# Kernel optimization log

Measured on AMD Instinct MI355X. Metric: run time of the kernel, lower is better.

Reference implementation:

```python
import jax, jax.numpy as jnp
import numpy as np

D_MODEL = 1024
D_STATE = 8          # max(8, 16 // 2)
D_CONV = 4
D_INNER = int(1.5 * D_MODEL)   # expand = max(1.5, 2*0.75)
DT_RANK = (D_MODEL + 15) // 16 # 64
D_FF = 2 * D_MODEL
B, L = 2, 2048


def layer_norm(x, g, b, eps=1e-5):
    mu = jnp.mean(x, -1, keepdims=True)
    var = jnp.var(x, -1, keepdims=True)
    return (x - mu) * jax.lax.rsqrt(var + eps) * g + b


def setup_inputs() -> dict:
    key = jax.random.key(0)
    ks = jax.random.split(key, 12)
    def n(k, shape, scale=0.02):
        return jax.random.normal(k, shape, dtype=jnp.float32) * scale
    return {
        'x': jax.random.normal(ks[0], (B, L, D_MODEL), dtype=jnp.float32),
        'ln1_g': jnp.ones((D_MODEL,), jnp.float32),
        'ln1_b': jnp.zeros((D_MODEL,), jnp.float32),
        'ln2_g': jnp.ones((D_MODEL,), jnp.float32),
        'ln2_b': jnp.zeros((D_MODEL,), jnp.float32),
        'in_proj_w': n(ks[1], (2 * D_INNER, D_MODEL)),
        'conv_w': n(ks[2], (D_INNER, 1, D_CONV), 0.1),
        'conv_b': jnp.zeros((D_INNER,), jnp.float32),
        'x_proj_w': n(ks[3], (DT_RANK + 2 * D_STATE, D_INNER)),
        'dt_proj_w': n(ks[4], (D_INNER, DT_RANK), 0.1),
        'dt_proj_b': n(ks[5], (D_INNER,), 0.1),
        'A_log': jnp.log(jnp.broadcast_to(jnp.arange(1, D_STATE + 1, dtype=jnp.float32), (D_INNER, D_STATE))),
        'D': jnp.ones((D_INNER,), jnp.float32),
        'out_proj_w': n(ks[6], (D_MODEL, D_INNER)),
        'ffn_w1': n(ks[7], (D_FF, D_MODEL)),
        'ffn_b1': jnp.zeros((D_FF,), jnp.float32),
        'ffn_w2': n(ks[8], (D_MODEL, D_FF)),
        'ffn_b2': jnp.zeros((D_MODEL,), jnp.float32),
    }


def mamba(x, in_proj_w, conv_w, conv_b, x_proj_w, dt_proj_w, dt_proj_b, A_log, Dp, out_proj_w):
    # in_proj -> (x, z)
    xz = x @ in_proj_w.T                       # (B, L, 2*d_inner)
    xi, z = jnp.split(xz, 2, axis=-1)
    # depthwise causal conv over seq, kernel 4
    xc = jnp.transpose(xi, (0, 2, 1))          # (B, d_inner, L)
    xc = jax.lax.conv_general_dilated(
        xc, conv_w, window_strides=(1,), padding=[(D_CONV - 1, 0)],
        dimension_numbers=('NCH', 'OIH', 'NCH'), feature_group_count=D_INNER)
    xc = xc + conv_b[None, :, None]
    u = jax.nn.silu(jnp.transpose(xc, (0, 2, 1)))  # (B, L, d_inner)
    # x_proj -> dt, B, C
    x_dbl = u @ x_proj_w.T
    dt = x_dbl[..., :DT_RANK]
    Bm = x_dbl[..., DT_RANK:DT_RANK + D_STATE]
    Cm = x_dbl[..., DT_RANK + D_STATE:]
    delta = jax.nn.softplus(dt @ dt_proj_w.T + dt_proj_b)  # (B, L, d_inner)
    A = -jnp.exp(A_log)                                    # (d_inner, d_state)
    dA = jnp.exp(jnp.einsum('bld,dn->bldn', delta, A))     # (B, L, d_inner, d_state)
    dBu = jnp.einsum('bld,bln,bld->bldn', delta, Bm, u)
    # selective scan over time
    def step(h, inputs):
        dA_t, dBu_t, C_t = inputs
        h = dA_t * h + dBu_t                   # (B, d_inner, d_state)
        y = jnp.einsum('bdn,bn->bd', h, C_t)
        return h, y
    h0 = jnp.zeros((x.shape[0], D_INNER, D_STATE), x.dtype)
    _, ys = jax.lax.scan(step, h0, (jnp.moveaxis(dA, 1, 0), jnp.moveaxis(dBu, 1, 0), jnp.moveaxis(Cm, 1, 0)))
    y = jnp.moveaxis(ys, 0, 1) + u * Dp        # skip connection D*u
    y = y * jax.nn.silu(z)                     # gate
    return y @ out_proj_w.T


def reference(x, ln1_g, ln1_b, ln2_g, ln2_b, in_proj_w, conv_w, conv_b, x_proj_w,
              dt_proj_w, dt_proj_b, A_log, D, out_proj_w, ffn_w1, ffn_b1, ffn_w2, ffn_b2):
    residual = x
    xp = layer_norm(x, ln1_g, ln1_b)
    x = mamba(xp, in_proj_w, conv_w, conv_b, x_proj_w, dt_proj_w, dt_proj_b, A_log, D, out_proj_w) + residual
    xn = layer_norm(x, ln2_g, ln2_b)
    h = jax.nn.gelu(xn @ ffn_w1.T + ffn_b1, approximate=False)  # dropout is identity in eval
    return x + (h @ ffn_w2.T + ffn_b2)
```

## Files before the change

kernel.cpp:

```cpp
#include <hip/hip_runtime.h>
#include <math.h>

#define D_MODEL 1024
#define D_STATE 8
#define D_CONV  4
#define D_INNER 1536
#define DT_RANK 64
#define D_FF    2048
#define BATCH   2
#define SEQ     2048
#define NROWS   (BATCH*SEQ)
#define NC      32
#define LC      (SEQ/NC)
#define XQW     512

typedef short bf16x8 __attribute__((ext_vector_type(8)));
typedef unsigned short u16x8 __attribute__((ext_vector_type(8)));
typedef float f32x4  __attribute__((ext_vector_type(4)));

__device__ inline unsigned short f2bf(float x) {
    union { float f; unsigned u; } v; v.f = x;
    unsigned r = v.u + 0x7fffu + ((v.u >> 16) & 1u);
    return (unsigned short)(r >> 16);
}
__device__ inline float bf2f(unsigned short h) {
    union { unsigned u; float f; } v; v.u = ((unsigned)h) << 16;
    return v.f;
}
__device__ inline float softplus_f(float x) {
    return (x > 20.0f) ? x : log1pf(__expf(x));
}
__device__ inline float gelu_f(float x) {
    return 0.5f * x * (1.0f + erff(x * 0.70710678118654752f));
}
__device__ inline float silu_f(float x) {
    return x / (1.0f + __expf(-x));
}
__device__ inline void gload16(const unsigned short* g, unsigned short* l) {
    typedef unsigned int u32;
    __builtin_amdgcn_global_load_lds(
        (const __attribute__((address_space(1))) u32*)g,
        (__attribute__((address_space(3))) u32*)l, 16, 0, 0);
}

#define PHASE_SYNC_PRE()  do { __builtin_amdgcn_s_barrier(); \
                               asm volatile("s_waitcnt lgkmcnt(0)" ::: "memory"); } while (0)
#define PHASE_SYNC_POST() do { __builtin_amdgcn_s_barrier(); } while (0)

__global__ __launch_bounds__(256) void prep_kernel(
    const float* __restrict__ s0, unsigned short* __restrict__ d0,
    const float* __restrict__ s1, unsigned short* __restrict__ d1,
    const float* __restrict__ s2, unsigned short* __restrict__ d2,
    const float* __restrict__ s3, unsigned short* __restrict__ d3,
    const float* __restrict__ s4, unsigned short* __restrict__ d4,
    const float* __restrict__ xpw, unsigned short* __restrict__ xpd,
    const float* __restrict__ x, const float* __restrict__ g1,
    const float* __restrict__ b1, unsigned short* __restrict__ xout) {
    int b = blockIdx.x;
    if (b < 4400) {
        const float* s; unsigned short* d; int base;
        if      (b < 1536) { s = s0; d = d0; base = b * 2048; }
        else if (b < 1584) { s = s1; d = d1; base = (b - 1536) * 2048; }
        else if (b < 2352) { s = s2; d = d2; base = (b - 1584) * 2048; }
        else if (b < 3376) { s = s3; d = d3; base = (b - 2352) * 2048; }
        else               { s = s4; d = d4; base = (b - 3376) * 2048; }
        int i = base + threadIdx.x * 8;
        float4 v0 = *(const float4*)(s + i);
        float4 v1 = *(const float4*)(s + i + 4);
        ushort4 a, c;
        a.x = f2bf(v0.x); a.y = f2bf(v0.y); a.z = f2bf(v0.z); a.w = f2bf(v0.w);
        c.x = f2bf(v1.x); c.y = f2bf(v1.y); c.z = f2bf(v1.z); c.w = f2bf(v1.w);
        *(ushort4*)(d + i)     = a;
        *(ushort4*)(d + i + 4) = c;
    } else if (b < 4528) {
        int row = b - 4400;
        for (int c = threadIdx.x; c < D_INNER; c += 256)
            xpd[row * D_INNER + c] = (row < 80) ? f2bf(xpw[row * D_INNER + c]) : (unsigned short)0;
    } else {
        __shared__ float sbuf[4];
        int row = b - 4528;
        int t = threadIdx.x;
        float4 v = ((const float4*)(x + (size_t)row * D_MODEL))[t];
        float s = v.x + v.y + v.z + v.w;
        for (int o = 32; o; o >>= 1) s += __shfl_down(s, o, 64);
        if ((t & 63) == 0) sbuf[t >> 6] = s;
        __syncthreads();
        float mu = (sbuf[0] + sbuf[1] + sbuf[2] + sbuf[3]) * (1.0f / D_MODEL);
        __syncthreads();
        float e0 = v.x - mu, e1 = v.y - mu, e2 = v.z - mu, e3 = v.w - mu;
        float q = e0*e0 + e1*e1 + e2*e2 + e3*e3;
        for (int o = 32; o; o >>= 1) q += __shfl_down(q, o, 64);
        if ((t & 63) == 0) sbuf[t >> 6] = q;
        __syncthreads();
        float var = (sbuf[0] + sbuf[1] + sbuf[2] + sbuf[3]) * (1.0f / D_MODEL);
        float rs = rsqrtf(var + 1e-5f);
        float4 gv = ((const float4*)g1)[t];
        float4 bv = ((const float4*)b1)[t];
        ushort4 st;
        st.x = f2bf(e0 * rs * gv.x + bv.x);
        st.y = f2bf(e1 * rs * gv.y + bv.y);
        st.z = f2bf(e2 * rs * gv.z + bv.z);
        st.w = f2bf(e3 * rs * gv.w + bv.w);
        ((ushort4*)(xout + (size_t)row * D_MODEL))[t] = st;
    }
}

#define EPI_F32        0
#define EPI_GELU_BF16  4
#define EPI_BF16       6
#define EPI_SOFTPLUS_BF16 7
#define EPI_PBF16      9

template<int WN, int EPI, int SPLITK>
__global__ __launch_bounds__(512, 2) void gemm8p(
    const unsigned short* __restrict__ A, int lda,
    const unsigned short* __restrict__ Bm, int ldb, int K,
    float* __restrict__ Cf, unsigned short* __restrict__ Cb, int ldc,
    const float* __restrict__ bias,
    const float* __restrict__ resid, int ldr) {
    constexpr int WM = 8 / WN;
    constexpr int BN = WN * 64;
    constexpr int RW = 256 / WM;
    constexpr int CW = 64;
    constexpr int MI = RW / 16;
    constexpr int NI = CW / 16;
    constexpr int MIH = MI / 2, NIH = NI / 2;
    constexpr int ABYTES = 256 * 128;
    constexpr int BBYTES = BN * 128;
    constexpr int BOFF = 2 * ABYTES;
    __shared__ unsigned short lds[(2 * ABYTES + 2 * BBYTES) / 2];

    const int t = threadIdx.x, l = t & 63, w = t >> 6;
    const int wr = w / WN, wc = w % WN;

    const int nx = gridDim.x;
    const int nwg = nx * gridDim.y;
    int bid = blockIdx.y * nx + blockIdx.x;
    int q = nwg >> 3;
    int swz = (bid & 7) * q + (bid >> 3);
    const int m0 = (swz / nx) * 256, n0 = (swz % nx) * BN;
    const int kbase = (SPLITK > 1) ? blockIdx.z * K : 0;

    const int sr = l >> 3;
    const int sj = ((l & 7) * 16) ^ ((l >> 3) << 4);
    const int row_l = w * 8;
    const int row_c = (w >> 2) * 64 + (w & 3) * 8;

    auto STG = [&](int bufbyte, int rowbase, const unsigned short* G, int ldg, int gbase, int kt) {
        unsigned short* dst = (unsigned short*)((char*)lds + bufbyte + rowbase * 128);
        const unsigned short* src = G + (size_t)(gbase + rowbase + sr) * ldg + kbase + kt * 64 + (sj >> 1);
        gload16(src, dst);
    };
    auto S_Ah0 = [&](int b, int kt) {
        if (WN == 4) { STG(b * ABYTES, row_l, A, lda, m0, kt);       STG(b * ABYTES, 128 + row_l, A, lda, m0, kt); }
        else         { STG(b * ABYTES, row_c, A, lda, m0, kt);       STG(b * ABYTES, 128 + row_c, A, lda, m0, kt); }
    };
    auto S_Ah1 = [&](int b, int kt) {
        if (WN == 4) { STG(b * ABYTES, 64 + row_l, A, lda, m0, kt);  STG(b * ABYTES, 192 + row_l, A, lda, m0, kt); }
        else         { STG(b * ABYTES, 32 + row_c, A, lda, m0, kt);  STG(b * ABYTES, 160 + row_c, A, lda, m0, kt); }
    };
    auto S_Bc0 = [&](int b, int kt) {
        if (WN == 4) { STG(BOFF + b * BBYTES, row_c, Bm, ldb, n0, kt); STG(BOFF + b * BBYTES, 128 + row_c, Bm, ldb, n0, kt); }
        else         { STG(BOFF + b * BBYTES, row_c, Bm, ldb, n0, kt); }
    };
    auto S_Bc1 = [&](int b, int kt) {
        if (WN == 4) { STG(BOFF + b * BBYTES, 32 + row_c, Bm, ldb, n0, kt); STG(BOFF + b * BBYTES, 160 + row_c, Bm, ldb, n0, kt); }
        else         { STG(BOFF + b * BBYTES, 32 + row_c, Bm, ldb, n0, kt); }
    };

    auto LD = [&](int bytebase, int row, int kb) -> bf16x8 {
        int o = bytebase + row * 128 + (kb ^ ((row & 7) << 4));
        return *(const bf16x8*)((const char*)lds + o);
    };

    f32x4 acc[MI][NI] = {};
    bf16x8 af[MIH][2], b0v[NIH][2], b1v[NIH][2];

    auto LDA_set = [&](int buf, int qr, auto& dst) {
        #pragma unroll
        for (int mi = 0; mi < MIH; mi++)
            #pragma unroll
            for (int ks = 0; ks < 2; ks++)
                dst[mi][ks] = LD(buf * ABYTES, wr * RW + qr * (RW / 2) + mi * 16 + (l & 15),
                                 ks * 64 + (l >> 4) * 16);
    };
    auto LDB_set = [&](int buf, int qc, auto& dst) {
        #pragma unroll
        for (int ni2 = 0; ni2 < NIH; ni2++)
            #pragma unroll
            for (int ks = 0; ks < 2; ks++)
                dst[ni2][ks] = LD(BOFF + buf * BBYTES, wc * CW + qc * 32 + ni2 * 16 + (l & 15),
                                  ks * 64 + (l >> 4) * 16);
    };
    auto MFMA_Q = [&](int qr, int qc, auto& a_, auto& b_) {
        __builtin_amdgcn_s_setprio(1);
        #pragma unroll
        for (int mi = 0; mi < MIH; mi++)
            #pragma unroll
            for (int ni2 = 0; ni2 < NIH; ni2++)
                #pragma unroll
                for (int ks = 0; ks < 2; ks++)
                    acc[qr * MIH + mi][qc * NIH + ni2] =
                        __builtin_amdgcn_mfma_f32_16x16x32_bf16(a_[mi][ks], b_[ni2][ks],
                                                                acc[qr * MIH + mi][qc * NIH + ni2], 0, 0, 0);
        __builtin_amdgcn_s_setprio(0);
    };
    auto VMW = [&](bool last) {
        if (last)            asm volatile("s_waitcnt vmcnt(0)" ::: "memory");
        else if (WN == 4)    asm volatile("s_waitcnt vmcnt(6)" ::: "memory");
        else                 asm volatile("s_waitcnt vmcnt(5)" ::: "memory");
    };

    const int ni_ = K >> 7;

    S_Ah0(0, 0); S_Ah1(0, 0); S_Bc0(0, 0); S_Bc1(0, 0);
    S_Ah0(1, 1); S_Ah1(1, 1); S_Bc0(1, 1); S_Bc1(1, 1);
    if (WN == 4) asm volatile("s_waitcnt vmcnt(8)" ::: "memory");
    else         asm volatile("s_waitcnt vmcnt(6)" ::: "memory");
    __builtin_amdgcn_s_barrier();

    for (int i = 0; i < ni_; i++) {
        const bool last = (i == ni_ - 1);
        const int t2 = 2 * i + 2, t3 = 2 * i + 3;
        LDA_set(0, 0, af); LDB_set(0, 0, b0v);
        if (i) S_Bc0(1, 2 * i + 1);
        PHASE_SYNC_PRE(); MFMA_Q(0, 0, af, b0v); PHASE_SYNC_POST();
        LDB_set(0, 1, b1v);
        if (!last) S_Ah0(0, t2);
        PHASE_SYNC_PRE(); MFMA_Q(0, 1, af, b1v); PHASE_SYNC_POST();
        LDA_set(0, 1, af);
        PHASE_SYNC_PRE(); MFMA_Q(1, 1, af, b1v); PHASE_SYNC_POST();
        LDB_set(0, 0, b0v);
        if (!last) { S_Ah1(0, t2); S_Bc1(0, t2); }
        VMW(last);
        PHASE_SYNC_PRE(); MFMA_Q(1, 0, af, b0v); PHASE_SYNC_POST();
        LDA_set(1, 0, af); LDB_set(1, 0, b0v);
        if (!last) S_Bc0(0, t2);
        PHASE_SYNC_PRE(); MFMA_Q(0, 0, af, b0v); PHASE_SYNC_POST();
        LDB_set(1, 1, b1v);
        if (!last) S_Ah0(1, t3);
        PHASE_SYNC_PRE(); MFMA_Q(0, 1, af, b1v); PHASE_SYNC_POST();
        LDA_set(1, 1, af);
        PHASE_SYNC_PRE(); MFMA_Q(1, 1, af, b1v); PHASE_SYNC_POST();
        LDB_set(1, 0, b0v);
        if (!last) { S_Ah1(1, t3); S_Bc1(1, t3); }
        VMW(last);
        PHASE_SYNC_PRE(); MFMA_Q(1, 0, af, b0v); PHASE_SYNC_POST();
    }

    float* Cfp = Cf;
    unsigned short* Cbp = Cb;
    if (SPLITK > 1) {
        Cfp += (size_t)blockIdx.z * NROWS * ldc;
        Cbp += (size_t)blockIdx.z * NROWS * ldc;
    }
    #pragma unroll
    for (int ni2 = 0; ni2 < NI; ni2++) {
        int col = n0 + wc * CW + ni2 * 16 + (l & 15);
        float bv = 0.0f;
        if (EPI == EPI_GELU_BF16) bv = bias[col];
        #pragma unroll
        for (int mi = 0; mi < MI; mi++) {
            #pragma unroll
            for (int j = 0; j < 4; j++) {
                int row = m0 + wr * RW + mi * 16 + (l >> 4) * 4 + j;
                float v = acc[mi][ni2][j];
                if (EPI == EPI_GELU_BF16)  v = gelu_f(v + bv);
                if (EPI == EPI_GELU_BF16 || EPI == EPI_BF16 || EPI == EPI_PBF16) {
                    Cbp[(size_t)row * ldc + col] = f2bf(v);
                } else {
                    Cfp[(size_t)row * ldc + col] = v;
                }
            }
        }
    }
}

__global__ __launch_bounds__(256) void sk2_ln(const unsigned short* __restrict__ p,
                                              const float* __restrict__ resid,
                                              const float* __restrict__ g,
                                              const float* __restrict__ b,
                                              float* __restrict__ x2,
                                              unsigned short* __restrict__ xn) {
    __shared__ float sbuf[4];
    int row = blockIdx.x;
    int t = threadIdx.x;
    const size_t seg = (size_t)NROWS * D_MODEL;
    size_t base = (size_t)row * D_MODEL + t * 4;
    ushort4 a = *(const ushort4*)(p + base);
    ushort4 bb = *(const ushort4*)(p + base + seg);
    float4 r = *(const float4*)(resid + base);
    float4 v;
    v.x = bf2f(a.x) + bf2f(bb.x) + r.x;
    v.y = bf2f(a.y) + bf2f(bb.y) + r.y;
    v.z = bf2f(a.z) + bf2f(bb.z) + r.z;
    v.w = bf2f(a.w) + bf2f(bb.w) + r.w;
    *(float4*)(x2 + base) = v;
    float s = v.x + v.y + v.z + v.w;
    for (int o = 32; o; o >>= 1) s += __shfl_down(s, o, 64);
    if ((t & 63) == 0) sbuf[t >> 6] = s;
    __syncthreads();
    float mu = (sbuf[0] + sbuf[1] + sbuf[2] + sbuf[3]) * (1.0f / D_MODEL);
    __syncthreads();
    float d0 = v.x - mu, d1 = v.y - mu, d2 = v.z - mu, d3 = v.w - mu;
    float qq = d0*d0 + d1*d1 + d2*d2 + d3*d3;
    for (int o = 32; o; o >>= 1) qq += __shfl_down(qq, o, 64);
    if ((t & 63) == 0) sbuf[t >> 6] = qq;
    __syncthreads();
    float var = (sbuf[0] + sbuf[1] + sbuf[2] + sbuf[3]) * (1.0f / D_MODEL);
    float rs = rsqrtf(var + 1e-5f);
    float4 gv = ((const float4*)g)[t];
    float4 bv = ((const float4*)b)[t];
    ushort4 st;
    st.x = f2bf(d0 * rs * gv.x + bv.x);
    st.y = f2bf(d1 * rs * gv.y + bv.y);
    st.z = f2bf(d2 * rs * gv.z + bv.z);
    st.w = f2bf(d3 * rs * gv.w + bv.w);
    ((ushort4*)(xn + (size_t)row * D_MODEL))[t] = st;
}

__global__ __launch_bounds__(256) void sk2_reduce(const unsigned short* __restrict__ p,
                                                  const float* __restrict__ bias,
                                                  const float* __restrict__ resid,
                                                  float* __restrict__ o) {
    int i = (blockIdx.x * 256 + threadIdx.x) * 4;
    const size_t seg = (size_t)NROWS * D_MODEL;
    ushort4 a = *(const ushort4*)(p + i);
    ushort4 b = *(const ushort4*)(p + i + seg);
    float4 r = *(const float4*)(resid + i);
    float4 bb = *(const float4*)(bias + (i & (D_MODEL - 1)));
    float4 o4;
    o4.x = bf2f(a.x) + bf2f(b.x) + r.x + bb.x;
    o4.y = bf2f(a.y) + bf2f(b.y) + r.y + bb.y;
    o4.z = bf2f(a.z) + bf2f(b.z) + r.z + bb.z;
    o4.w = bf2f(a.w) + bf2f(b.w) + r.w + bb.w;
    *(float4*)(o + i) = o4;
}

__global__ __launch_bounds__(256) void xproj_conv_gemm(
    const unsigned short* __restrict__ xz, const float* __restrict__ cw,
    const float* __restrict__ cb, unsigned short* __restrict__ u,
    const unsigned short* __restrict__ B,
    unsigned short* __restrict__ xq) {
    __shared__ unsigned short As[128 * 32];
    __shared__ unsigned short Bs[128 * 32];
    int t = threadIdx.x, l = t & 63, w = t >> 6;
    int m0 = blockIdx.x * 128;
    int kbase = blockIdx.y * 384;
    int c0 = 2 * w, c1 = 2 * w + 1;
    int srow = l >> 2, scol = (l & 3) * 8;
    const unsigned short* Bg0 = B + (size_t)(16 * c0 + srow) * D_INNER + kbase + scol;
    const unsigned short* Bg1 = B + (size_t)(16 * c1 + srow) * D_INNER + kbase + scol;
    int wr = w >> 1, wc = w & 1;
    int aoff = (wr * 64 + (l & 15)) * 32 + (l >> 4) * 8;
    int boff = (wc * 64 + (l & 15)) * 32 + (l >> 4) * 8;

    f32x4 acc[4][4] = {};

    for (int ti = 0; ti < 12; ti++) {
        int k0 = ti * 32;
        gload16(Bg0 + k0, &Bs[c0 * 512]);
        gload16(Bg1 + k0, &Bs[c1 * 512]);
        #pragma unroll
        for (int cc = 0; cc < 2; cc++) {
            int ch = 2 * w + cc;
            int bl = m0 + 16 * ch + srow;
            int d0 = kbase + k0 + scol;
            int lq = bl & (SEQ - 1);
            u16x8 rr[4];
            #pragma unroll
            for (int kk = 0; kk < 4; kk++) {
                if (lq - 3 + kk >= 0)
                    rr[kk] = *(const u16x8*)(xz + (size_t)(bl - 3 + kk) * (2 * D_INNER) + d0);
                else
                    rr[kk] = (u16x8)0;
            }
            float4 cb0 = *(const float4*)(cb + d0);
            float4 cb1 = *(const float4*)(cb + d0 + 4);
            float av[8];
            av[0] = cb0.x; av[1] = cb0.y; av[2] = cb0.z; av[3] = cb0.w;
            av[4] = cb1.x; av[5] = cb1.y; av[6] = cb1.z; av[7] = cb1.w;
            u16x8 o;
            #pragma unroll
            for (int j = 0; j < 8; j++) {
                float4 wv = *(const float4*)(cw + (d0 + j) * 4);
                float s = av[j];
                s += bf2f((unsigned short)rr[0][j]) * wv.x;
                s += bf2f((unsigned short)rr[1][j]) * wv.y;
                s += bf2f((unsigned short)rr[2][j]) * wv.z;
                s += bf2f((unsigned short)rr[3][j]) * wv.w;
                o[j] = f2bf(silu_f(s));
            }
            *(u16x8*)(&As[ch * 512 + l * 8]) = o;
            *(u16x8*)(u + (size_t)bl * D_INNER + d0) = o;
        }
        __syncthreads();
        bf16x8 af[4], bfv[4];
        #pragma unroll
        for (int i = 0; i < 4; i++) af[i] = *(const bf16x8*)(&As[aoff + i * 512]);
        #pragma unroll
        for (int i = 0; i < 4; i++) bfv[i] = *(const bf16x8*)(&Bs[boff + i * 512]);
        __builtin_amdgcn_s_setprio(1);
        #pragma unroll
        for (int mi = 0; mi < 4; mi++)
            #pragma unroll
            for (int ni = 0; ni < 4; ni++)
                acc[mi][ni] = __builtin_amdgcn_mfma_f32_16x16x32_bf16(af[mi], bfv[ni], acc[mi][ni], 0, 0, 0);
        __builtin_amdgcn_s_setprio(0);
        __syncthreads();
    }

    unsigned short* Cb = xq + blockIdx.y * 128;
    int colb = wc * 64 + (l & 15);
    int rowb = m0 + wr * 64 + (l >> 4) * 4;
    #pragma unroll
    for (int ni = 0; ni < 4; ni++) {
        int col = colb + ni * 16;
        #pragma unroll
        for (int mi = 0; mi < 4; mi++) {
            #pragma unroll
            for (int j = 0; j < 4; j++) {
                int row = rowb + mi * 16 + j;
                Cb[(size_t)row * XQW + col] = f2bf(acc[mi][ni][j]);
            }
        }
    }
}

__global__ __launch_bounds__(256) void xdt_reduce(const unsigned short* __restrict__ xq,
                                                  unsigned short* __restrict__ xdt) {
    int i = blockIdx.x * 256 + threadIdx.x;
    int row = i >> 4;
    int c = (i & 15) * 4;
    const unsigned short* xr = xq + (size_t)row * XQW + c;
    ushort4 a0 = *(const ushort4*)(xr);
    ushort4 a1 = *(const ushort4*)(xr + 128);
    ushort4 a2 = *(const ushort4*)(xr + 256);
    ushort4 a3 = *(const ushort4*)(xr + 384);
    ushort4 o;
    o.x = f2bf(bf2f(a0.x) + bf2f(a1.x) + bf2f(a2.x) + bf2f(a3.x));
    o.y = f2bf(bf2f(a0.y) + bf2f(a1.y) + bf2f(a2.y) + bf2f(a3.y));
    o.z = f2bf(bf2f(a0.z) + bf2f(a1.z) + bf2f(a2.z) + bf2f(a3.z));
    o.w = f2bf(bf2f(a0.w) + bf2f(a1.w) + bf2f(a2.w) + bf2f(a3.w));
    *(ushort4*)(xdt + (size_t)row * DT_RANK + c) = o;
}

template<int EPI>
__global__ __launch_bounds__(256) void gemm_mfma(
    const unsigned short* __restrict__ A, int lda,
    const unsigned short* __restrict__ B, int ldb, int K,
    float* __restrict__ Cf, unsigned short* __restrict__ Cb, int ldc,
    const float* __restrict__ bias) {
    __shared__ unsigned short As[3][128 * 32];
    __shared__ unsigned short Bs[3][128 * 32];
    int t = threadIdx.x, l = t & 63, w = t >> 6;
    int nx = gridDim.x;
    int nwg = nx * gridDim.y;
    int bid = blockIdx.y * nx + blockIdx.x;
    int q = nwg >> 3;
    int swz = (bid & 7) * q + (bid >> 3);
    int m0 = (swz / nx) * 128, n0 = (swz % nx) * 128;
    int c0 = 2 * w, c1 = 2 * w + 1;
    int srow = l >> 2, scol = (l & 3) * 8;
    const unsigned short* Ag0 = A + (size_t)(m0 + 16 * c0 + srow) * lda + scol;
    const unsigned short* Ag1 = A + (size_t)(m0 + 16 * c1 + srow) * lda + scol;
    const unsigned short* Bg0 = B + (size_t)(n0 + 16 * c0 + srow) * ldb + scol;
    const unsigned short* Bg1 = B + (size_t)(n0 + 16 * c1 + srow) * ldb + scol;
    int wr = w >> 1, wc = w & 1;
    int aoff = (wr * 64 + (l & 15)) * 32 + (l >> 4) * 8;
    int boff = (wc * 64 + (l & 15)) * 32 + (l >> 4) * 8;

    f32x4 acc[4][4] = {};
    int nt = K >> 5;

    gload16(Ag0, &As[0][c0 * 512]);
    gload16(Ag1, &As[0][c1 * 512]);
    gload16(Bg0, &Bs[0][c0 * 512]);
    gload16(Bg1, &Bs[0][c1 * 512]);
    if (nt > 1) {
        gload16(Ag0 + 32, &As[1][c0 * 512]);
        gload16(Ag1 + 32, &As[1][c1 * 512]);
        gload16(Bg0 + 32, &Bs[1][c0 * 512]);
        gload16(Bg1 + 32, &Bs[1][c1 * 512]);
    }

    int cur = 0;
    for (int ti = 0; ti < nt; ti++) {
        int pf = ti + 2;
        if (pf < nt) {
            int nb = cur - 1; if (nb < 0) nb += 3;
            int k0 = pf << 5;
            gload16(Ag0 + k0, &As[nb][c0 * 512]);
            gload16(Ag1 + k0, &As[nb][c1 * 512]);
            gload16(Bg0 + k0, &Bs[nb][c0 * 512]);
            gload16(Bg1 + k0, &Bs[nb][c1 * 512]);
        }
        int rem = nt - 1 - ti;
        if (rem >= 2)      asm volatile("s_waitcnt vmcnt(8)" ::: "memory");
        else if (rem == 1) asm volatile("s_waitcnt vmcnt(4)" ::: "memory");
        else               asm volatile("s_waitcnt vmcnt(0)" ::: "memory");
        __builtin_amdgcn_s_barrier();

        const unsigned short* Ab = &As[cur][0];
        const unsigned short* Bb = &Bs[cur][0];
        bf16x8 af[4], bfv[4];
        #pragma unroll
        for (int i = 0; i < 4; i++) af[i] = *(const bf16x8*)(Ab + aoff + i * 512);
        #pragma unroll
        for (int i = 0; i < 4; i++) bfv[i] = *(const bf16x8*)(Bb + boff + i * 512);
        __builtin_amdgcn_s_setprio(1);
        #pragma unroll
        for (int mi = 0; mi < 4; mi++)
            #pragma unroll
            for (int ni = 0; ni < 4; ni++)
                acc[mi][ni] = __builtin_amdgcn_mfma_f32_16x16x32_bf16(af[mi], bfv[ni], acc[mi][ni], 0, 0, 0);
        __builtin_amdgcn_s_setprio(0);
        __builtin_amdgcn_s_barrier();
        cur++; if (cur == 3) cur = 0;
    }

    int colb = n0 + wc * 64 + (l & 15);
    int rowb = m0 + wr * 64 + (l >> 4) * 4;
    #pragma unroll
    for (int ni = 0; ni < 4; ni++) {
        int col = colb + ni * 16;
        float bv = 0.0f;
        if (EPI == EPI_SOFTPLUS_BF16) bv = bias[col];
        #pragma unroll
        for (int mi = 0; mi < 4; mi++) {
            #pragma unroll
            for (int j = 0; j < 4; j++) {
                int row = rowb + mi * 16 + j;
                float v = acc[mi][ni][j];
                if (EPI == EPI_SOFTPLUS_BF16) v = softplus_f(v + bv);
                if (EPI == EPI_BF16 || EPI == EPI_SOFTPLUS_BF16) {
                    Cb[(size_t)row * ldc + col] = f2bf(v);
                } else {
                    Cf[(size_t)row * ldc + col] = v;
                }
            }
        }
    }
}

__global__ __launch_bounds__(256) void scan_passA(const unsigned short* __restrict__ delta,
                                                  const unsigned short* __restrict__ u,
                                                  const unsigned short* __restrict__ xq,
                                                  const float* __restrict__ A_log,
                                                  float* __restrict__ P,
                                                  float* __restrict__ S) {
    int d = blockIdx.x * 256 + threadIdx.x;
    int c = blockIdx.y, b = blockIdx.z;
    __shared__ float bc[LC][16];
    int base_row = b * SEQ + c * LC;
    for (int e = threadIdx.x; e < LC * 16; e += 256) {
        int lrr = e >> 4, col = e & 15;
        const unsigned short* xr = xq + (size_t)(base_row + lrr) * XQW + 64 + col;
        bc[lrr][col] = bf2f(xr[0]) + bf2f(xr[128]) + bf2f(xr[256]) + bf2f(xr[384]);
    }
    __syncthreads();
    float Ad[8];
    #pragma unroll
    for (int n = 0; n < 8; n++) Ad[n] = -__expf(A_log[d * 8 + n]);
    float prod[8], hs[8];
    #pragma unroll
    for (int n = 0; n < 8; n++) { prod[n] = 1.0f; hs[n] = 0.0f; }
    for (int lrr = 0; lrr < LC; lrr++) {
        int row = base_row + lrr;
        float dl = bf2f(delta[(size_t)row * D_INNER + d]);
        float uu = bf2f(u[(size_t)row * D_INNER + d]);
        float du = dl * uu;
        #pragma unroll
        for (int n = 0; n < 8; n++) {
            float dA = __expf(dl * Ad[n]);
            prod[n] *= dA;
            hs[n] = dA * hs[n] + du * bc[lrr][n];
        }
    }
    size_t o = ((size_t)((size_t)b * NC + c) * D_INNER + d) * 8;
    #pragma unroll
    for (int n = 0; n < 8; n++) { P[o + n] = prod[n]; S[o + n] = hs[n]; }
}

__global__ __launch_bounds__(256) void scan_passB(const float* __restrict__ P,
                                                  const float* __restrict__ S,
                                                  float* __restrict__ hstart) {
    int tid = blockIdx.x * 256 + threadIdx.x;
    int b = tid / (D_INNER * 8);
    int rem = tid % (D_INNER * 8);
    float h = 0.0f;
    for (int c = 0; c < NC; c++) {
        size_t o = (size_t)(b * NC + c) * (D_INNER * 8) + rem;
        hstart[o] = h;
        h = P[o] * h + S[o];
    }
}

__global__ __launch_bounds__(256) void scan_passC(const unsigned short* __restrict__ delta,
                                                  const unsigned short* __restrict__ u,
                                                  const unsigned short* __restrict__ xq,
                                                  const float* __restrict__ A_log,
                                                  const float* __restrict__ hstart,
                                                  const unsigned short* __restrict__ xz,
                                                  const float* __restrict__ Dp,
                                                  unsigned short* __restrict__ ygate) {
    int d = blockIdx.x * 256 + threadIdx.x;
    int c = blockIdx.y, b = blockIdx.z;
    __shared__ float bc[LC][16];
    int base_row = b * SEQ + c * LC;
    for (int e = threadIdx.x; e < LC * 16; e += 256) {
        int lrr = e >> 4, col = e & 15;
        const unsigned short* xr = xq + (size_t)(base_row + lrr) * XQW + 64 + col;
        bc[lrr][col] = bf2f(xr[0]) + bf2f(xr[128]) + bf2f(xr[256]) + bf2f(xr[384]);
    }
    __syncthreads();
    float Ad[8];
    #pragma unroll
    for (int n = 0; n < 8; n++) Ad[n] = -__expf(A_log[d * 8 + n]);
    float h[8];
    size_t ho = ((size_t)((size_t)b * NC + c) * D_INNER + d) * 8;
    #pragma unroll
    for (int n = 0; n < 8; n++) h[n] = hstart[ho + n];
    float Dd = Dp[d];
    for (int lrr = 0; lrr < LC; lrr++) {
        int row = base_row + lrr;
        float dl = bf2f(delta[(size_t)row * D_INNER + d]);
        float uu = bf2f(u[(size_t)row * D_INNER + d]);
        float du = dl * uu;
        float y = 0.0f;
        #pragma unroll
        for (int n = 0; n < 8; n++) {
            float dA = __expf(dl * Ad[n]);
            h[n] = dA * h[n] + du * bc[lrr][n];
            y += h[n] * bc[lrr][8 + n];
        }
        y += uu * Dd;
        float z = bf2f(xz[(size_t)row * (2 * D_INNER) + D_INNER + d]);
        ygate[(size_t)row * D_INNER + d] = f2bf(y * silu_f(z));
    }
}

extern "C" void kernel_launch(void* const* d_in, const int* in_sizes, int n_in,
                              void* d_out, int out_size, void* d_ws, size_t ws_size,
                              hipStream_t stream) {
    const float* x         = (const float*)d_in[0];
    const float* ln1_g     = (const float*)d_in[1];
    const float* ln1_b     = (const float*)d_in[2];
    const float* ln2_g     = (const float*)d_in[3];
    const float* ln2_b     = (const float*)d_in[4];
    const float* in_proj_w = (const float*)d_in[5];
    const float* conv_w    = (const float*)d_in[6];
    const float* conv_b    = (const float*)d_in[7];
    const float* x_proj_w  = (const float*)d_in[8];
    const float* dt_proj_w = (const float*)d_in[9];
    const float* dt_proj_b = (const float*)d_in[10];
    const float* A_log     = (const float*)d_in[11];
    const float* Dp        = (const float*)d_in[12];
    const float* out_proj_w= (const float*)d_in[13];
    const float* ffn_w1    = (const float*)d_in[14];
    const float* ffn_b1    = (const float*)d_in[15];
    const float* ffn_w2    = (const float*)d_in[16];
    const float* ffn_b2    = (const float*)d_in[17];
    float* out = (float*)d_out;

    float* P     = (float*)d_ws;
    float* S     = P + (size_t)BATCH * NC * D_INNER * 8;
    float* hst   = S + (size_t)BATCH * NC * D_INNER * 8;
    float* x2    = hst + (size_t)BATCH * NC * D_INNER * 8;
    unsigned short* psum_bf = (unsigned short*)(x2 + (size_t)NROWS * D_MODEL);
    unsigned short* xq      = psum_bf + 2 * (size_t)NROWS * D_MODEL;
    unsigned short* xdt_bf  = xq + (size_t)NROWS * XQW;
    unsigned short* xz_bf   = xdt_bf + (size_t)NROWS * DT_RANK;
    unsigned short* xp_bf   = xz_bf + (size_t)NROWS * 2 * D_INNER;
    unsigned short* u_bf    = xp_bf + (size_t)NROWS * D_MODEL;
    unsigned short* yg_bf   = u_bf + (size_t)NROWS * D_INNER;
    unsigned short* dl_bf   = yg_bf + (size_t)NROWS * D_INNER;
    unsigned short* w_in    = dl_bf + (size_t)NROWS * D_INNER;
    unsigned short* w_xp    = w_in + (size_t)2 * D_INNER * D_MODEL;
    unsigned short* w_dt    = w_xp + (size_t)128 * D_INNER;
    unsigned short* w_out   = w_dt + (size_t)D_INNER * DT_RANK;
    unsigned short* w_f1    = w_out + (size_t)D_MODEL * D_INNER;
    unsigned short* w_f2    = w_f1 + (size_t)D_FF * D_MODEL;
    unsigned short* hff_bf  = xz_bf;

    prep_kernel<<<4528 + NROWS, 256, 0, stream>>>(
        in_proj_w, w_in, dt_proj_w, w_dt, out_proj_w, w_out, ffn_w1, w_f1, ffn_w2, w_f2,
        x_proj_w, w_xp, x, ln1_g, ln1_b, xp_bf);
    gemm8p<4, EPI_BF16, 1><<<dim3(3072 / 256, NROWS / 256), 512, 0, stream>>>(
        xp_bf, D_MODEL, w_in, D_MODEL, D_MODEL, nullptr, xz_bf, 2 * D_INNER, nullptr, nullptr, 0);
    xproj_conv_gemm<<<dim3(NROWS / 128, 4), 256, 0, stream>>>(
        xz_bf, conv_w, conv_b, u_bf, w_xp, xq);
    xdt_reduce<<<(NROWS * 16) / 256, 256, 0, stream>>>(xq, xdt_bf);
    gemm_mfma<EPI_SOFTPLUS_BF16><<<dim3(D_INNER / 128, NROWS / 128), 256, 0, stream>>>(
        xdt_bf, DT_RANK, w_dt, DT_RANK, DT_RANK, nullptr, dl_bf, D_INNER, dt_proj_b);
    scan_passA<<<dim3(D_INNER / 256, NC, BATCH), 256, 0, stream>>>(dl_bf, u_bf, xq, A_log, P, S);
    scan_passB<<<(BATCH * D_INNER * 8) / 256, 256, 0, stream>>>(P, S, hst);
    scan_passC<<<dim3(D_INNER / 256, NC, BATCH), 256, 0, stream>>>(dl_bf, u_bf, xq, A_log, hst, xz_bf, Dp, yg_bf);
    gemm8p<2, EPI_PBF16, 2><<<dim3(D_MODEL / 128, NROWS / 256, 2), 512, 0, stream>>>(
        yg_bf, D_INNER, w_out, D_INNER, D_INNER / 2, nullptr, psum_bf, D_MODEL, nullptr, nullptr, 0);
    sk2_ln<<<NROWS, 256, 0, stream>>>(psum_bf, x, ln2_g, ln2_b, x2, xp_bf);
    gemm8p<2, EPI_GELU_BF16, 1><<<dim3(D_FF / 128, NROWS / 256), 512, 0, stream>>>(
        xp_bf, D_MODEL, w_f1, D_MODEL, D_MODEL, nullptr, hff_bf, D_FF, ffn_b1, nullptr, 0);
    gemm8p<2, EPI_PBF16, 2><<<dim3(D_MODEL / 128, NROWS / 256, 2), 512, 0, stream>>>(
        hff_bf, D_FF, w_f2, D_FF, D_FF / 2, nullptr, psum_bf, D_MODEL, nullptr, nullptr, 0);
    sk2_reduce<<<(NROWS * D_MODEL) / 1024, 256, 0, stream>>>(psum_bf, ffn_b2, x2, out);
}
```

Measured before the change: 268.0 us.

## Fuse dt split-K reduce into dt_proj GEMM; add 4-phase GEMM schedule

Removes the standalone xdt_reduce kernel. The four bf16 partial sums of the x_proj dt slice are now reduced while being staged into shared memory inside a new dt_fused kernel. That kernel loads the whole K=64 at once and applies the softplus-plus-bias epilogue, which saves one launch and the round trip of the xdt intermediate. It also adds a 4-phase variant of the gemm8p main loop, which issues two MFMA quadrants per sync phase and uses adjusted vmcnt waits, and uses it for the WN=2 GEMMs. The 4-phase loop cuts barrier overhead but may reduce overlap between memory traffic and compute.

```diff
diff --git a/kernel.cpp b/kernel.cpp
--- a/kernel.cpp
+++ b/kernel.cpp
@@ -111,7 +111,7 @@
 #define EPI_SOFTPLUS_BF16 7
 #define EPI_PBF16      9
 
-template<int WN, int EPI, int SPLITK>
+template<int WN, int EPI, int SPLITK, int PH>
 __global__ __launch_bounds__(512, 2) void gemm8p(
     const unsigned short* __restrict__ A, int lda,
     const unsigned short* __restrict__ Bm, int ldb, int K,
@@ -205,10 +205,15 @@
                                                                 acc[qr * MIH + mi][qc * NIH + ni2], 0, 0, 0);
         __builtin_amdgcn_s_setprio(0);
     };
-    auto VMW = [&](bool last) {
+    auto VMW8 = [&](bool last) {
         if (last)            asm volatile("s_waitcnt vmcnt(0)" ::: "memory");
         else if (WN == 4)    asm volatile("s_waitcnt vmcnt(6)" ::: "memory");
         else                 asm volatile("s_waitcnt vmcnt(5)" ::: "memory");
+    };
+    auto VMW4 = [&](bool last) {
+        if (last)            asm volatile("s_waitcnt vmcnt(0)" ::: "memory");
+        else if (WN == 4)    asm volatile("s_waitcnt vmcnt(4)" ::: "memory");
+        else                 asm volatile("s_waitcnt vmcnt(3)" ::: "memory");
     };
 
     const int ni_ = K >> 7;
@@ -219,33 +224,62 @@
     else         asm volatile("s_waitcnt vmcnt(6)" ::: "memory");
     __builtin_amdgcn_s_barrier();
 
-    for (int i = 0; i < ni_; i++) {
-        const bool last = (i == ni_ - 1);
-        const int t2 = 2 * i + 2, t3 = 2 * i + 3;
-        LDA_set(0, 0, af); LDB_set(0, 0, b0v);
-        if (i) S_Bc0(1, 2 * i + 1);
-        PHASE_SYNC_PRE(); MFMA_Q(0, 0, af, b0v); PHASE_SYNC_POST();
-        LDB_set(0, 1, b1v);
-        if (!last) S_Ah0(0, t2);
-        PHASE_SYNC_PRE(); MFMA_Q(0, 1, af, b1v); PHASE_SYNC_POST();
-        LDA_set(0, 1, af);
-        PHASE_SYNC_PRE(); MFMA_Q(1, 1, af, b1v); PHASE_SYNC_POST();
-        LDB_set(0, 0, b0v);
-        if (!last) { S_Ah1(0, t2); S_Bc1(0, t2); }
-        VMW(last);
-        PHASE_SYNC_PRE(); MFMA_Q(1, 0, af, b0v); PHASE_SYNC_POST();
-        LDA_set(1, 0, af); LDB_set(1, 0, b0v);
-        if (!last) S_Bc0(0, t2);
-        PHASE_SYNC_PRE(); MFMA_Q(0, 0, af, b0v); PHASE_SYNC_POST();
-        LDB_set(1, 1, b1v);
-        if (!last) S_Ah0(1, t3);
-        PHASE_SYNC_PRE(); MFMA_Q(0, 1, af, b1v); PHASE_SYNC_POST();
-        LDA_set(1, 1, af);
-        PHASE_SYNC_PRE(); MFMA_Q(1, 1, af, b1v); PHASE_SYNC_POST();
-        LDB_set(1, 0, b0v);
-        if (!last) { S_Ah1(1, t3); S_Bc1(1, t3); }
-        VMW(last);
-        PHASE_SYNC_PRE(); MFMA_Q(1, 0, af, b0v); PHASE_SYNC_POST();
+    if constexpr (PH == 8) {
+        for (int i = 0; i < ni_; i++) {
+            const bool last = (i == ni_ - 1);
+            const int t2 = 2 * i + 2, t3 = 2 * i + 3;
+            LDA_set(0, 0, af); LDB_set(0, 0, b0v);
+            if (i) S_Bc0(1, 2 * i + 1);
+            PHASE_SYNC_PRE(); MFMA_Q(0, 0, af, b0v); PHASE_SYNC_POST();
+            LDB_set(0, 1, b1v);
+            if (!last) S_Ah0(0, t2);
+            PHASE_SYNC_PRE(); MFMA_Q(0, 1, af, b1v); PHASE_SYNC_POST();
+            LDA_set(0, 1, af);
+            PHASE_SYNC_PRE(); MFMA_Q(1, 1, af, b1v); PHASE_SYNC_POST();
+            LDB_set(0, 0, b0v);
+            if (!last) { S_Ah1(0, t2); S_Bc1(0, t2); }
+            VMW8(last);
+            PHASE_SYNC_PRE(); MFMA_Q(1, 0, af, b0v); PHASE_SYNC_POST();
+            LDA_set(1, 0, af); LDB_set(1, 0, b0v);
+            if (!last) S_Bc0(0, t2);
+            PHASE_SYNC_PRE(); MFMA_Q(0, 0, af, b0v); PHASE_SYNC_POST();
+            LDB_set(1, 1, b1v);
+            if (!last) S_Ah0(1, t3);
+            PHASE_SYNC_PRE(); MFMA_Q(0, 1, af, b1v); PHASE_SYNC_POST();
+            LDA_set(1, 1, af);
+            PHASE_SYNC_PRE(); MFMA_Q(1, 1, af, b1v); PHASE_SYNC_POST();
+            LDB_set(1, 0, b0v);
+            if (!last) { S_Ah1(1, t3); S_Bc1(1, t3); }
+            VMW8(last);
+            PHASE_SYNC_PRE(); MFMA_Q(1, 0, af, b0v); PHASE_SYNC_POST();
+        }
+    } else {
+        for (int i = 0; i < ni_; i++) {
+            const bool last = (i == ni_ - 1);
+            const int t2 = 2 * i + 2, t3 = 2 * i + 3;
+            LDA_set(0, 0, af); LDB_set(0, 0, b0v); LDB_set(0, 1, b1v);
+            if (i) { S_Bc0(1, 2 * i + 1); S_Ah1(1, 2 * i + 1); }
+            PHASE_SYNC_PRE();
+            MFMA_Q(0, 0, af, b0v); MFMA_Q(0, 1, af, b1v);
+            PHASE_SYNC_POST();
+            LDA_set(0, 1, af);
+            if (!last) { S_Ah0(0, t2); S_Bc1(0, t2); }
+            VMW4(last);
+            PHASE_SYNC_PRE();
+            MFMA_Q(1, 1, af, b1v); MFMA_Q(1, 0, af, b0v);
+            PHASE_SYNC_POST();
+            LDA_set(1, 0, af); LDB_set(1, 0, b0v); LDB_set(1, 1, b1v);
+            if (!last) { S_Bc0(0, t2); S_Ah1(0, t2); }
+            PHASE_SYNC_PRE();
+            MFMA_Q(0, 0, af, b0v); MFMA_Q(0, 1, af, b1v);
+            PHASE_SYNC_POST();
+            LDA_set(1, 1, af);
+            if (!last) { S_Ah0(1, t3); S_Bc1(1, t3); }
+            VMW4(last);
+            PHASE_SYNC_PRE();
+            MFMA_Q(1, 1, af, b1v); MFMA_Q(1, 0, af, b0v);
+            PHASE_SYNC_POST();
+        }
     }
 
     float* Cfp = Cf;
@@ -427,32 +461,13 @@
     }
 }
 
-__global__ __launch_bounds__(256) void xdt_reduce(const unsigned short* __restrict__ xq,
-                                                  unsigned short* __restrict__ xdt) {
-    int i = blockIdx.x * 256 + threadIdx.x;
-    int row = i >> 4;
-    int c = (i & 15) * 4;
-    const unsigned short* xr = xq + (size_t)row * XQW + c;
-    ushort4 a0 = *(const ushort4*)(xr);
-    ushort4 a1 = *(const ushort4*)(xr + 128);
-    ushort4 a2 = *(const ushort4*)(xr + 256);
-    ushort4 a3 = *(const ushort4*)(xr + 384);
-    ushort4 o;
-    o.x = f2bf(bf2f(a0.x) + bf2f(a1.x) + bf2f(a2.x) + bf2f(a3.x));
-    o.y = f2bf(bf2f(a0.y) + bf2f(a1.y) + bf2f(a2.y) + bf2f(a3.y));
-    o.z = f2bf(bf2f(a0.z) + bf2f(a1.z) + bf2f(a2.z) + bf2f(a3.z));
-    o.w = f2bf(bf2f(a0.w) + bf2f(a1.w) + bf2f(a2.w) + bf2f(a3.w));
-    *(ushort4*)(xdt + (size_t)row * DT_RANK + c) = o;
-}
-
-template<int EPI>
-__global__ __launch_bounds__(256) void gemm_mfma(
-    const unsigned short* __restrict__ A, int lda,
-    const unsigned short* __restrict__ B, int ldb, int K,
-    float* __restrict__ Cf, unsigned short* __restrict__ Cb, int ldc,
-    const float* __restrict__ bias) {
-    __shared__ unsigned short As[3][128 * 32];
-    __shared__ unsigned short Bs[3][128 * 32];
+__global__ __launch_bounds__(256) void dt_fused(
+    const unsigned short* __restrict__ xq,
+    const unsigned short* __restrict__ wdt,
+    const float* __restrict__ bias,
+    unsigned short* __restrict__ dl) {
+    __shared__ unsigned short As[2][128 * 32];
+    __shared__ unsigned short Bs[2][128 * 32];
     int t = threadIdx.x, l = t & 63, w = t >> 6;
     int nx = gridDim.x;
     int nwg = nx * gridDim.y;
@@ -462,82 +477,61 @@
     int m0 = (swz / nx) * 128, n0 = (swz % nx) * 128;
     int c0 = 2 * w, c1 = 2 * w + 1;
     int srow = l >> 2, scol = (l & 3) * 8;
-    const unsigned short* Ag0 = A + (size_t)(m0 + 16 * c0 + srow) * lda + scol;
-    const unsigned short* Ag1 = A + (size_t)(m0 + 16 * c1 + srow) * lda + scol;
-    const unsigned short* Bg0 = B + (size_t)(n0 + 16 * c0 + srow) * ldb + scol;
-    const unsigned short* Bg1 = B + (size_t)(n0 + 16 * c1 + srow) * ldb + scol;
+    #pragma unroll
+    for (int kc = 0; kc < 2; kc++) {
+        gload16(wdt + (size_t)(n0 + 16 * c0 + srow) * 64 + kc * 32 + scol, &Bs[kc][c0 * 512]);
+        gload16(wdt + (size_t)(n0 + 16 * c1 + srow) * 64 + kc * 32 + scol, &Bs[kc][c1 * 512]);
+    }
+    #pragma unroll
+    for (int kc = 0; kc < 2; kc++) {
+        #pragma unroll
+        for (int cc = 0; cc < 2; cc++) {
+            int ch = 2 * w + cc;
+            int row = m0 + 16 * ch + srow;
+            int col = kc * 32 + scol;
+            const unsigned short* xr = xq + (size_t)row * XQW + col;
+            u16x8 a0 = *(const u16x8*)(xr);
+            u16x8 a1 = *(const u16x8*)(xr + 128);
+            u16x8 a2 = *(const u16x8*)(xr + 256);
+            u16x8 a3 = *(const u16x8*)(xr + 384);
+            u16x8 o;
+            #pragma unroll
+            for (int j = 0; j < 8; j++)
+                o[j] = f2bf(bf2f((unsigned short)a0[j]) + bf2f((unsigned short)a1[j]) +
+                            bf2f((unsigned short)a2[j]) + bf2f((unsigned short)a3[j]));
+            *(u16x8*)(&As[kc][ch * 512 + l * 8]) = o;
+        }
+    }
+    __syncthreads();
     int wr = w >> 1, wc = w & 1;
     int aoff = (wr * 64 + (l & 15)) * 32 + (l >> 4) * 8;
     int boff = (wc * 64 + (l & 15)) * 32 + (l >> 4) * 8;
-
     f32x4 acc[4][4] = {};
-    int nt = K >> 5;
-
-    gload16(Ag0, &As[0][c0 * 512]);
-    gload16(Ag1, &As[0][c1 * 512]);
-    gload16(Bg0, &Bs[0][c0 * 512]);
-    gload16(Bg1, &Bs[0][c1 * 512]);
-    if (nt > 1) {
-        gload16(Ag0 + 32, &As[1][c0 * 512]);
-        gload16(Ag1 + 32, &As[1][c1 * 512]);
-        gload16(Bg0 + 32, &Bs[1][c0 * 512]);
-        gload16(Bg1 + 32, &Bs[1][c1 * 512]);
-    }
-
-    int cur = 0;
-    for (int ti = 0; ti < nt; ti++) {
-        int pf = ti + 2;
-        if (pf < nt) {
-            int nb = cur - 1; if (nb < 0) nb += 3;
-            int k0 = pf << 5;
-            gload16(Ag0 + k0, &As[nb][c0 * 512]);
-            gload16(Ag1 + k0, &As[nb][c1 * 512]);
-            gload16(Bg0 + k0, &Bs[nb][c0 * 512]);
-            gload16(Bg1 + k0, &Bs[nb][c1 * 512]);
-        }
-        int rem = nt - 1 - ti;
-        if (rem >= 2)      asm volatile("s_waitcnt vmcnt(8)" ::: "memory");
-        else if (rem == 1) asm volatile("s_waitcnt vmcnt(4)" ::: "memory");
-        else               asm volatile("s_waitcnt vmcnt(0)" ::: "memory");
-        __builtin_amdgcn_s_barrier();
-
-        const unsigned short* Ab = &As[cur][0];
-        const unsigned short* Bb = &Bs[cur][0];
+    #pragma unroll
+    for (int kc = 0; kc < 2; kc++) {
         bf16x8 af[4], bfv[4];
         #pragma unroll
-        for (int i = 0; i < 4; i++) af[i] = *(const bf16x8*)(Ab + aoff + i * 512);
-        #pragma unroll
-        for (int i = 0; i < 4; i++) bfv[i] = *(const bf16x8*)(Bb + boff + i * 512);
-        __builtin_amdgcn_s_setprio(1);
+        for (int i = 0; i < 4; i++) af[i] = *(const bf16x8*)(&As[kc][aoff + i * 512]);
+        #pragma unroll
+        for (int i = 0; i < 4; i++) bfv[i] = *(const bf16x8*)(&Bs[kc][boff + i * 512]);
         #pragma unroll
         for (int mi = 0; mi < 4; mi++)
             #pragma unroll
             for (int ni = 0; ni < 4; ni++)
                 acc[mi][ni] = __builtin_amdgcn_mfma_f32_16x16x32_bf16(af[mi], bfv[ni], acc[mi][ni], 0, 0, 0);
-        __builtin_amdgcn_s_setprio(0);
-        __builtin_amdgcn_s_barrier();
-        cur++; if (cur == 3) cur = 0;
-    }
-
+    }
     int colb = n0 + wc * 64 + (l & 15);
     int rowb = m0 + wr * 64 + (l >> 4) * 4;
     #pragma unroll
     for (int ni = 0; ni < 4; ni++) {
         int col = colb + ni * 16;
-        float bv = 0.0f;
-        if (EPI == EPI_SOFTPLUS_BF16) bv = bias[col];
+        float bv = bias[col];
         #pragma unroll
         for (int mi = 0; mi < 4; mi++) {
             #pragma unroll
             for (int j = 0; j < 4; j++) {
                 int row = rowb + mi * 16 + j;
-                float v = acc[mi][ni][j];
-                if (EPI == EPI_SOFTPLUS_BF16) v = softplus_f(v + bv);
-                if (EPI == EPI_BF16 || EPI == EPI_SOFTPLUS_BF16) {
-                    Cb[(size_t)row * ldc + col] = f2bf(v);
-                } else {
-                    Cf[(size_t)row * ldc + col] = v;
-                }
+                dl[(size_t)row * D_INNER + col] = f2bf(softplus_f(acc[mi][ni][j] + bv));
             }
         }
     }
@@ -669,8 +663,7 @@
     float* x2    = hst + (size_t)BATCH * NC * D_INNER * 8;
     unsigned short* psum_bf = (unsigned short*)(x2 + (size_t)NROWS * D_MODEL);
     unsigned short* xq      = psum_bf + 2 * (size_t)NROWS * D_MODEL;
-    unsigned short* xdt_bf  = xq + (size_t)NROWS * XQW;
-    unsigned short* xz_bf   = xdt_bf + (size_t)NROWS * DT_RANK;
+    unsigned short* xz_bf   = xq + (size_t)NROWS * XQW;
     unsigned short* xp_bf   = xz_bf + (size_t)NROWS * 2 * D_INNER;
     unsigned short* u_bf    = xp_bf + (size_t)NROWS * D_MODEL;
     unsigned short* yg_bf   = u_bf + (size_t)NROWS * D_INNER;
@@ -686,22 +679,21 @@
     prep_kernel<<<4528 + NROWS, 256, 0, stream>>>(
         in_proj_w, w_in, dt_proj_w, w_dt, out_proj_w, w_out, ffn_w1, w_f1, ffn_w2, w_f2,
         x_proj_w, w_xp, x, ln1_g, ln1_b, xp_bf);
-    gemm8p<4, EPI_BF16, 1><<<dim3(3072 / 256, NROWS / 256), 512, 0, stream>>>(
+    gemm8p<4, EPI_BF16, 1, 8><<<dim3(3072 / 256, NROWS / 256), 512, 0, stream>>>(
         xp_bf, D_MODEL, w_in, D_MODEL, D_MODEL, nullptr, xz_bf, 2 * D_INNER, nullptr, nullptr, 0);
     xproj_conv_gemm<<<dim3(NROWS / 128, 4), 256, 0, stream>>>(
         xz_bf, conv_w, conv_b, u_bf, w_xp, xq);
-    xdt_reduce<<<(NROWS * 16) / 256, 256, 0, stream>>>(xq, xdt_bf);
-    gemm_mfma<EPI_SOFTPLUS_BF16><<<dim3(D_INNER / 128, NROWS / 128), 256, 0, stream>>>(
-        xdt_bf, DT_RANK, w_dt, DT_RANK, DT_RANK, nullptr, dl_bf, D_INNER, dt_proj_b);
+    dt_fused<<<dim3(D_INNER / 128, NROWS / 128), 256, 0, stream>>>(
+        xq, w_dt, dt_proj_b, dl_bf);
     scan_passA<<<dim3(D_INNER / 256, NC, BATCH), 256, 0, stream>>>(dl_bf, u_bf, xq, A_log, P, S);
     scan_passB<<<(BATCH * D_INNER * 8) / 256, 256, 0, stream>>>(P, S, hst);
     scan_passC<<<dim3(D_INNER / 256, NC, BATCH), 256, 0, stream>>>(dl_bf, u_bf, xq, A_log, hst, xz_bf, Dp, yg_bf);
-    gemm8p<2, EPI_PBF16, 2><<<dim3(D_MODEL / 128, NROWS / 256, 2), 512, 0, stream>>>(
+    gemm8p<2, EPI_PBF16, 2, 4><<<dim3(D_MODEL / 128, NROWS / 256, 2), 512, 0, stream>>>(
         yg_bf, D_INNER, w_out, D_INNER, D_INNER / 2, nullptr, psum_bf, D_MODEL, nullptr, nullptr, 0);
     sk2_ln<<<NROWS, 256, 0, stream>>>(psum_bf, x, ln2_g, ln2_b, x2, xp_bf);
-    gemm8p<2, EPI_GELU_BF16, 1><<<dim3(D_FF / 128, NROWS / 256), 512, 0, stream>>>(
+    gemm8p<2, EPI_GELU_BF16, 1, 4><<<dim3(D_FF / 128, NROWS / 256), 512, 0, stream>>>(
         xp_bf, D_MODEL, w_f1, D_MODEL, D_MODEL, nullptr, hff_bf, D_FF, ffn_b1, nullptr, 0);
-    gemm8p<2, EPI_PBF16, 2><<<dim3(D_MODEL / 128, NROWS / 256, 2), 512, 0, stream>>>(
+    gemm8p<2, EPI_PBF16, 2, 4><<<dim3(D_MODEL / 128, NROWS / 256, 2), 512, 0, stream>>>(
         hff_bf, D_FF, w_f2, D_FF, D_FF / 2, nullptr, psum_bf, D_MODEL, nullptr, nullptr, 0);
     sk2_reduce<<<(NROWS * D_MODEL) / 1024, 256, 0, stream>>>(psum_bf, ffn_b2, x2, out);
 }
```

Result: no change. 265.9 us (-0.8%).
